# Kernel tuning notes

Hardware: AMD Instinct MI355X
Metric: run time of the kernel (lower is better)

The kernel has to match this reference:

```python
import jax, jax.numpy as jnp
import numpy as np

TOP_K = 2
CAPACITY_FACTOR = 1.0


def _ffn(x, w1, w2):
    # SwiGLU FFN: x [N, D], w1 [D, 2F], w2 [F, D]
    h = x @ w1
    x1, x2 = jnp.split(h, 2, axis=-1)
    return (x1 * jax.nn.silu(x2)) @ w2


def setup_inputs() -> dict:
    key = jax.random.key(0)
    ks = jax.random.split(key, 6)
    B, S, D, F, E_r, E_s = 4, 2048, 2048, 1024, 7, 1
    sc_in = 1.0 / np.sqrt(D)
    sc_mid = 1.0 / np.sqrt(F)
    return {
        "x": jax.random.normal(ks[0], (B, S, D), dtype=jnp.float32),
        "gate_w": jax.random.normal(ks[1], (D, E_r), dtype=jnp.float32) * sc_in,
        "expert_bias": jnp.zeros((E_r,), dtype=jnp.float32),
        "shared_w1": jax.random.normal(ks[2], (E_s, D, 2 * F), dtype=jnp.float32) * sc_in,
        "shared_w2": jax.random.normal(ks[3], (E_s, F, D), dtype=jnp.float32) * sc_mid,
        "routed_w1": jax.random.normal(ks[4], (E_r, D, 2 * F), dtype=jnp.float32) * sc_in,
        "routed_w2": jax.random.normal(ks[5], (E_r, F, D), dtype=jnp.float32) * sc_mid,
    }


def reference(x, gate_w, expert_bias, shared_w1, shared_w2, routed_w1, routed_w2):
    B, S, D = x.shape
    E_r = gate_w.shape[1]
    T = B * S
    capacity = max(1, int(CAPACITY_FACTOR * T / E_r))
    flat_x = x.reshape(T, D)

    # shared experts: applied to every token, summed
    shared_sum = jax.vmap(_ffn, in_axes=(None, 0, 0))(flat_x, shared_w1, shared_w2).sum(0)

    # gating (eval mode: no noise, no dropout)
    gate_logits = flat_x @ gate_w + expert_bias  # [T, E_r]
    aff = jax.nn.sigmoid(gate_logits)
    _, topk_idx = jax.lax.top_k(aff, TOP_K)  # [T, K]
    # mask[t, e] = expert e is among token t's top-k
    mask = (topk_idx[:, :, None] == jnp.arange(E_r)[None, None, :]).any(axis=1)  # [T, E_r]

    # per-expert capacity selection: keep top-`capacity` masked tokens by affinity
    score = jnp.where(mask, aff, -1.0).T  # [E_r, T]; aff >= 0 so -1 sorts last
    _, sel_idx = jax.lax.top_k(score, capacity)  # [E_r, capacity] token ids
    kept = jnp.take_along_axis(mask.T, sel_idx, axis=1)  # [E_r, cap]
    w = jnp.where(kept, jnp.take_along_axis(aff.T, sel_idx, axis=1), 0.0)  # [E_r, cap]

    # grouped gather -> FFN -> weighted scatter-add
    inp = flat_x[sel_idx]  # [E_r, cap, D]
    out = jax.vmap(_ffn)(inp, routed_w1, routed_w2)  # [E_r, cap, D]
    routed_sum = jnp.zeros_like(flat_x).at[sel_idx].add(out * w[:, :, None])

    return (shared_sum + routed_sum).reshape(B, S, D)
```

## Files before the change

### kernel.cpp

```cpp
#include <hip/hip_runtime.h>
#include <hip/hip_bf16.h>

typedef unsigned long long u64;
typedef __bf16 bf16x8 __attribute__((ext_vector_type(8)));
typedef float f32x4 __attribute__((ext_vector_type(4)));
typedef unsigned short ushort8_t __attribute__((ext_vector_type(8)));

#define TOKS 8192
#define DMODEL 2048
#define FD 1024
#define NEXP 7
#define CAP 1170
#define CAPP 1280

#define MFMA16(a, b, c) __builtin_amdgcn_mfma_f32_16x16x32_bf16(a, b, c, 0, 0, 0)

__device__ __forceinline__ unsigned short f2bf(float f) {
  __hip_bfloat16 b = __float2bfloat16(f);
  return __builtin_bit_cast(unsigned short, b);
}
__device__ __forceinline__ float bf2f(unsigned short u) {
  __hip_bfloat16 b = __builtin_bit_cast(__hip_bfloat16, u);
  return __bfloat162float(b);
}
__device__ __forceinline__ void gload_lds16(const void* g, void* l) {
  __builtin_amdgcn_global_load_lds(
      (const __attribute__((address_space(1))) void*)g,
      (__attribute__((address_space(3))) void*)l, 16, 0, 0);
}

__global__ void k_convert_x(const float* __restrict__ x,
                            unsigned short* __restrict__ xb, long n4) {
  long i = (long)blockIdx.x * blockDim.x + threadIdx.x;
  long stride = (long)gridDim.x * blockDim.x;
  for (; i < n4; i += stride) {
    float4 v = ((const float4*)x)[i];
    ushort4 o;
    o.x = f2bf(v.x); o.y = f2bf(v.y); o.z = f2bf(v.z); o.w = f2bf(v.w);
    ((ushort4*)xb)[i] = o;
  }
}

template <bool PERM>
__global__ void k_transpose_bf16(const float* __restrict__ in0,
                                 const float* __restrict__ inr,
                                 unsigned short* __restrict__ out,
                                 int R, int C) {
  __shared__ float tile[32][33];
  int z = blockIdx.z;
  const float* in = (z == 0) ? in0 : (inr + (long)(z - 1) * R * C);
  unsigned short* o = out + (long)z * R * C;
  int c0 = blockIdx.x * 32;
  int r0 = blockIdx.y * 32;
  int tx = threadIdx.x, ty = threadIdx.y;
#pragma unroll
  for (int k = 0; k < 4; ++k)
    tile[ty + 8 * k][tx] = in[(long)(r0 + ty + 8 * k) * C + c0 + tx];
  __syncthreads();
#pragma unroll
  for (int k = 0; k < 4; ++k) {
    int c = c0 + ty + 8 * k;
    long orow = PERM ? (long)(((c & 1023) >> 4) * 32 + ((c >> 10) << 4) + (c & 15))
                     : (long)c;
    o[orow * R + r0 + tx] = f2bf(tile[tx][ty + 8 * k]);
  }
}

__global__ void k_gating(const float* __restrict__ x,
                         const float* __restrict__ gw,
                         const float* __restrict__ bias,
                         u64* __restrict__ keys) {
  int wave = threadIdx.x >> 6;
  int lane = threadIdx.x & 63;
  int t = blockIdx.x * 4 + wave;
  const float* xr = x + (long)t * DMODEL;
  double acc[NEXP];
#pragma unroll
  for (int e = 0; e < NEXP; ++e) acc[e] = 0.0;
  for (int i = lane; i < DMODEL; i += 64) {
    double xv = (double)xr[i];
    const float* g = gw + (long)i * NEXP;
#pragma unroll
    for (int e = 0; e < NEXP; ++e) acc[e] += xv * (double)g[e];
  }
#pragma unroll
  for (int e = 0; e < NEXP; ++e) {
    for (int off = 32; off > 0; off >>= 1)
      acc[e] += __shfl_down(acc[e], off, 64);
  }
  if (lane == 0) {
    float aff[NEXP];
#pragma unroll
    for (int e = 0; e < NEXP; ++e) {
      double lg = acc[e] + (double)bias[e];
      aff[e] = (float)(1.0 / (1.0 + exp(-lg)));
    }
    int i1 = 0;
    for (int e = 1; e < NEXP; ++e) if (aff[e] > aff[i1]) i1 = e;
    int i2 = -1;
    for (int e = 0; e < NEXP; ++e) {
      if (e == i1) continue;
      if (i2 < 0 || aff[e] > aff[i2]) i2 = e;
    }
#pragma unroll
    for (int e = 0; e < NEXP; ++e) {
      u64 key = (u64)(0xFFFFFFFFu - (unsigned)t);
      if (e == i1 || e == i2) key |= ((u64)__float_as_uint(aff[e])) << 32;
      keys[(long)e * TOKS + t] = key;
    }
  }
}

__global__ __launch_bounds__(1024) void k_select(
    const u64* __restrict__ keys, int* __restrict__ sel,
    float* __restrict__ selw, unsigned* __restrict__ cnt,
    int* __restrict__ inv) {
  __shared__ unsigned hist[256];
  __shared__ u64 s_prefix;
  __shared__ unsigned s_k;
  __shared__ unsigned s_cnt;
  const int e = blockIdx.x;
  const u64* kk = keys + (long)e * TOKS;
  const int tid = threadIdx.x;
  if (tid == 0) { s_prefix = 0; s_k = CAP; s_cnt = 0; }
  __syncthreads();
  for (int shift = 56; shift >= 0; shift -= 8) {
    if (tid < 256) hist[tid] = 0;
    __syncthreads();
    u64 pref = s_prefix;
    for (int i = tid; i < TOKS; i += 1024) {
      u64 key = kk[i];
      bool match = (shift == 56) || ((key >> (shift + 8)) == pref);
      if (match) atomicAdd(&hist[(unsigned)(key >> shift) & 255u], 1u);
    }
    __syncthreads();
    if (tid == 0) {
      unsigned k = s_k, cum = 0;
      for (int b = 255; b >= 0; --b) {
        unsigned c = hist[b];
        if (cum + c >= k) {
          s_prefix = (s_prefix << 8) | (unsigned)b;
          s_k = k - cum;
          break;
        }
        cum += c;
      }
    }
    __syncthreads();
  }
  const u64 T = s_prefix;
  for (int i = tid; i < TOKS; i += 1024) {
    u64 key = kk[i];
    if (key >= T) {
      unsigned p = atomicAdd(&s_cnt, 1u);
      int tok = (int)(0xFFFFFFFFu - (unsigned)(key & 0xFFFFFFFFull));
      unsigned vb = (unsigned)(key >> 32);
      sel[e * CAPP + p] = tok;
      selw[e * CAPP + p] = vb ? __uint_as_float(vb) : 0.0f;
      if (vb) {
        unsigned pos = atomicAdd(&cnt[tok], 1u);
        inv[tok * 2 + pos] = e * CAPP + (int)p;
      }
    }
  }
  for (int i = CAP + tid; i < CAPP; i += 1024) {
    sel[e * CAPP + i] = 0;
    selw[e * CAPP + i] = 0.0f;
  }
}

__global__ __launch_bounds__(256) void k_combine(
    float* __restrict__ out, const unsigned short* __restrict__ rout,
    const int* __restrict__ inv, const unsigned* __restrict__ cnt) {
  const int tok = blockIdx.x;
  const unsigned c = cnt[tok];
  if (c == 0) return;
  int i0 = inv[tok * 2];
  int i1 = (c > 1) ? inv[tok * 2 + 1] : -1;
  if (c > 1 && i1 < i0) { int t = i0; i0 = i1; i1 = t; }
  const int col = threadIdx.x * 8;
  float* o = out + (long)tok * DMODEL + col;
  float4 v0 = *(float4*)o;
  float4 v1 = *(float4*)(o + 4);
  ushort8_t r0 = *(const ushort8_t*)&rout[(long)i0 * DMODEL + col];
#pragma unroll
  for (int j = 0; j < 4; ++j) { v0.x; }
  v0.x += bf2f(r0[0]); v0.y += bf2f(r0[1]); v0.z += bf2f(r0[2]); v0.w += bf2f(r0[3]);
  v1.x += bf2f(r0[4]); v1.y += bf2f(r0[5]); v1.z += bf2f(r0[6]); v1.w += bf2f(r0[7]);
  if (c > 1) {
    ushort8_t r1 = *(const ushort8_t*)&rout[(long)i1 * DMODEL + col];
    v0.x += bf2f(r1[0]); v0.y += bf2f(r1[1]); v0.z += bf2f(r1[2]); v0.w += bf2f(r1[3]);
    v1.x += bf2f(r1[4]); v1.y += bf2f(r1[5]); v1.z += bf2f(r1[6]); v1.w += bf2f(r1[7]);
  }
  *(float4*)o = v0;
  *(float4*)(o + 4) = v1;
}

template <int EPI, bool GATHER>
__global__ __launch_bounds__(256, 4) void k_gemm128(
    const unsigned short* __restrict__ Abase,
    const unsigned short* __restrict__ Bbase,
    unsigned short* __restrict__ Cbf, float* __restrict__ Cf32,
    const int* __restrict__ sel, const float* __restrict__ selw,
    int N, int K, long strideA, long strideB, long strideC) {
  __shared__ unsigned short lds[2][8192];
  const int tid = threadIdx.x;
  const int w = tid >> 6;
  const int lane = tid & 63;

  long lin = blockIdx.x + (long)gridDim.x * (blockIdx.y + (long)gridDim.y * blockIdx.z);
  long nwg = (long)gridDim.x * gridDim.y * gridDim.z;
  long swz = (lin & 7) * (nwg >> 3) + (lin >> 3);
  int bx = (int)(swz % gridDim.x);
  long rem = swz / gridDim.x;
  int by = (int)(rem % gridDim.y);
  int z = (int)(rem / gridDim.y);

  const long m0 = (long)by * 128;
  const long n0 = (long)bx * 128;
  const unsigned short* A = Abase + (GATHER ? 0L : (long)z * strideA);
  const unsigned short* Bm = Bbase + (long)z * strideB;

  const int wr = w >> 1;
  const int wc = w & 1;
  const int lr = lane & 15;
  const int kq = lane >> 4;

  const int r_ = (w << 4) + (lane >> 2);
  const int p_ = lane & 3;
  const unsigned short* aSrc[2];
  const unsigned short* bSrc[2];
#pragma unroll
  for (int c = 0; c < 2; ++c) {
    int r = c * 64 + r_;
    int q = p_ ^ ((r & 3) ^ ((r >> 2) & 3));
    long ar = GATHER ? (long)sel[z * CAPP + (int)m0 + r] : (m0 + r);
    aSrc[c] = A + ar * (long)K + q * 8;
    bSrc[c] = Bm + (n0 + r) * (long)K + q * 8;
  }
  const int dst0 = tid * 8;

  auto STAGE = [&](int buf, int t) {
    const long ko = (long)t * 32;
#pragma unroll
    for (int c = 0; c < 2; ++c) {
      gload_lds16(aSrc[c] + ko, &lds[buf][c * 2048 + dst0]);
      gload_lds16(bSrc[c] + ko, &lds[buf][4096 + c * 2048 + dst0]);
    }
  };

  const int gl = (lr & 3) ^ ((lr >> 2) & 3);
  const int slot = (kq ^ gl) * 8;
  const int aRow = wr * 64 + lr;
  const int bRow = wc * 64 + lr;

  const int nk = K >> 5;

  STAGE(0, 0);
  asm volatile("s_waitcnt vmcnt(0)" ::: "memory");
  __builtin_amdgcn_sched_barrier(0);
  __builtin_amdgcn_s_barrier();
  __builtin_amdgcn_sched_barrier(0);

  f32x4 acc[4][4] = {};
  int cur = 0;

#pragma unroll 1
  for (int t = 0; t < nk; ++t) {
    if (t + 1 < nk) STAGE(cur ^ 1, t + 1);
    const unsigned short* aSeg = &lds[cur][0];
    const unsigned short* bSeg = &lds[cur][4096];
    bf16x8 af[4], bf[4];
#pragma unroll
    for (int m = 0; m < 4; ++m)
      af[m] = *(const bf16x8*)&aSeg[(aRow + m * 16) * 32 + slot];
#pragma unroll
    for (int n = 0; n < 4; ++n)
      bf[n] = *(const bf16x8*)&bSeg[(bRow + n * 16) * 32 + slot];
    asm volatile("s_waitcnt lgkmcnt(0)" ::: "memory");
    __builtin_amdgcn_sched_barrier(0);
    __builtin_amdgcn_s_setprio(1);
#pragma unroll
    for (int m = 0; m < 4; ++m)
#pragma unroll
      for (int n = 0; n < 4; ++n)
        acc[m][n] = MFMA16(af[m], bf[n], acc[m][n]);
    __builtin_amdgcn_s_setprio(0);
    asm volatile("s_waitcnt vmcnt(0)" ::: "memory");
    __builtin_amdgcn_sched_barrier(0);
    __builtin_amdgcn_s_barrier();
    __builtin_amdgcn_sched_barrier(0);
    cur ^= 1;
  }

  const int r0q = (lane >> 4) * 4;
  const int cc = lane & 15;
  const long crow0 = m0 + wr * 64;
  const long ccol0 = n0 + wc * 64;

  if (EPI == 1) {
#pragma unroll
    for (int m = 0; m < 4; ++m)
#pragma unroll
      for (int r = 0; r < 4; ++r) {
        long row = crow0 + m * 16 + r0q + r;
#pragma unroll
        for (int n = 0; n < 4; ++n)
          Cf32[row * N + ccol0 + n * 16 + cc] = acc[m][n][r];
      }
  } else if (EPI == 3) {
    unsigned short* C = Cbf + (long)z * strideC;
    const int halfN = N >> 1;
    const long gcol0 = (ccol0 >> 1);
#pragma unroll
    for (int m = 0; m < 4; ++m)
#pragma unroll
      for (int r = 0; r < 4; ++r) {
        long row = crow0 + m * 16 + r0q + r;
#pragma unroll
        for (int q = 0; q < 2; ++q) {
          float x1v = acc[m][2 * q][r];
          float x2v = acc[m][2 * q + 1][r];
          float s = x2v / (1.0f + __expf(-x2v));
          C[row * halfN + gcol0 + q * 16 + cc] = f2bf(x1v * s);
        }
      }
  } else {
#pragma unroll
    for (int m = 0; m < 4; ++m)
#pragma unroll
      for (int r = 0; r < 4; ++r) {
        int rloc = (int)crow0 + m * 16 + r0q + r;
        float wgt = selw[z * CAPP + rloc];
        unsigned short* C = Cbf + ((long)z * CAPP + rloc) * N;
#pragma unroll
        for (int n = 0; n < 4; ++n)
          C[ccol0 + n * 16 + cc] = f2bf(acc[m][n][r] * wgt);
      }
  }
}

extern "C" void kernel_launch(void* const* d_in, const int* in_sizes, int n_in,
                              void* d_out, int out_size, void* d_ws,
                              size_t ws_size, hipStream_t stream) {
  (void)in_sizes; (void)n_in; (void)out_size; (void)ws_size;
  const float* x = (const float*)d_in[0];
  const float* gw = (const float*)d_in[1];
  const float* eb = (const float*)d_in[2];
  const float* sw1 = (const float*)d_in[3];
  const float* sw2 = (const float*)d_in[4];
  const float* rw1 = (const float*)d_in[5];
  const float* rw2 = (const float*)d_in[6];
  float* out = (float*)d_out;

  char* ws = (char*)d_ws;
  size_t off = 0;
  auto alloc = [&](size_t bytes) {
    size_t o = off;
    off += (bytes + 255) & ~(size_t)255;
    return o;
  };
  unsigned short* xb  = (unsigned short*)(ws + alloc((size_t)TOKS * DMODEL * 2));
  unsigned short* w1t = (unsigned short*)(ws + alloc((size_t)8 * DMODEL * (2 * FD) * 2));
  unsigned short* w2t = (unsigned short*)(ws + alloc((size_t)8 * DMODEL * FD * 2));
  unsigned short* a_sh = (unsigned short*)(ws + alloc((size_t)TOKS * FD * 2));
  unsigned short* a_r  = (unsigned short*)(ws + alloc((size_t)NEXP * CAPP * FD * 2));
  unsigned short* r_out = (unsigned short*)(ws + alloc((size_t)NEXP * CAPP * DMODEL * 2));
  u64* keys = (u64*)(ws + alloc((size_t)NEXP * TOKS * 8));
  int* sel  = (int*)(ws + alloc((size_t)NEXP * CAPP * 4));
  float* selw = (float*)(ws + alloc((size_t)NEXP * CAPP * 4));
  unsigned* cnt = (unsigned*)(ws + alloc((size_t)TOKS * 4));
  int* inv = (int*)(ws + alloc((size_t)TOKS * 2 * 4));

  k_convert_x<<<8192, 256, 0, stream>>>(x, xb, (long)TOKS * DMODEL / 4);
  dim3 tb(32, 8);
  k_transpose_bf16<true><<<dim3(64, 64, 8), tb, 0, stream>>>(sw1, rw1, w1t, DMODEL, 2 * FD);
  k_transpose_bf16<false><<<dim3(64, 32, 8), tb, 0, stream>>>(sw2, rw2, w2t, FD, DMODEL);
  k_gating<<<TOKS / 4, 256, 0, stream>>>(x, gw, eb, keys);
  hipMemsetAsync(cnt, 0, (size_t)TOKS * 4, stream);
  k_select<<<NEXP, 1024, 0, stream>>>(keys, sel, selw, cnt, inv);
  k_gemm128<3, false><<<dim3(16, 64, 1), 256, 0, stream>>>(
      xb, w1t, a_sh, nullptr, nullptr, nullptr, 2 * FD, DMODEL, 0, 0, 0);
  k_gemm128<1, false><<<dim3(16, 64, 1), 256, 0, stream>>>(
      a_sh, w2t, nullptr, out, nullptr, nullptr, DMODEL, FD, 0, 0, 0);
  k_gemm128<3, true><<<dim3(16, CAPP / 128, NEXP), 256, 0, stream>>>(
      xb, w1t + (size_t)DMODEL * (2 * FD), a_r, nullptr, sel, nullptr, 2 * FD,
      DMODEL, 0, (long)DMODEL * (2 * FD), (long)CAPP * FD);
  k_gemm128<4, false><<<dim3(16, CAPP / 128, NEXP), 256, 0, stream>>>(
      a_r, w2t + (size_t)DMODEL * FD, r_out, nullptr, sel, selw, DMODEL, FD,
      (long)CAPP * FD, (long)DMODEL * FD, 0);
  k_combine<<<TOKS, 256, 0, stream>>>(out, r_out, inv, cnt);
}
```

Measured before the change: 518.3 us.

## Merge shared and routed FFN GEMMs into unified launches; fuse convert with gating

```diff
diff --git a/kernel.cpp b/kernel.cpp
--- a/kernel.cpp
+++ b/kernel.cpp
@@ -12,6 +12,7 @@
 #define NEXP 7
 #define CAP 1170
 #define CAPP 1280
+#define URT 134
 
 #define MFMA16(a, b, c) __builtin_amdgcn_mfma_f32_16x16x32_bf16(a, b, c, 0, 0, 0)
 
@@ -29,15 +30,61 @@
       (__attribute__((address_space(3))) void*)l, 16, 0, 0);
 }
 
-__global__ void k_convert_x(const float* __restrict__ x,
-                            unsigned short* __restrict__ xb, long n4) {
-  long i = (long)blockIdx.x * blockDim.x + threadIdx.x;
-  long stride = (long)gridDim.x * blockDim.x;
-  for (; i < n4; i += stride) {
-    float4 v = ((const float4*)x)[i];
-    ushort4 o;
-    o.x = f2bf(v.x); o.y = f2bf(v.y); o.z = f2bf(v.z); o.w = f2bf(v.w);
-    ((ushort4*)xb)[i] = o;
+__global__ __launch_bounds__(256) void k_conv_gate(
+    const float* __restrict__ x, const float* __restrict__ gw,
+    const float* __restrict__ bias, unsigned short* __restrict__ xb,
+    u64* __restrict__ keys) {
+  const int t = blockIdx.x;
+  const int tid = threadIdx.x;
+  const int lane = tid & 63, wv = tid >> 6;
+  const float* xr = x + (long)t * DMODEL;
+  const int i0 = tid * 8;
+  float4 v0 = *(const float4*)&xr[i0];
+  float4 v1 = *(const float4*)&xr[i0 + 4];
+  float xv[8] = {v0.x, v0.y, v0.z, v0.w, v1.x, v1.y, v1.z, v1.w};
+  ushort8_t o;
+#pragma unroll
+  for (int j = 0; j < 8; ++j) o[j] = f2bf(xv[j]);
+  *(ushort8_t*)&xb[(long)t * DMODEL + i0] = o;
+  double acc[NEXP];
+#pragma unroll
+  for (int e = 0; e < NEXP; ++e) acc[e] = 0.0;
+#pragma unroll
+  for (int j = 0; j < 8; ++j) {
+    const float* g = gw + (long)(i0 + j) * NEXP;
+    double xd = (double)xv[j];
+#pragma unroll
+    for (int e = 0; e < NEXP; ++e) acc[e] += xd * (double)g[e];
+  }
+#pragma unroll
+  for (int e = 0; e < NEXP; ++e)
+    for (int off = 32; off > 0; off >>= 1)
+      acc[e] += __shfl_down(acc[e], off, 64);
+  __shared__ double red[4][NEXP];
+  if (lane == 0)
+#pragma unroll
+    for (int e = 0; e < NEXP; ++e) red[wv][e] = acc[e];
+  __syncthreads();
+  if (tid == 0) {
+    float aff[NEXP];
+#pragma unroll
+    for (int e = 0; e < NEXP; ++e) {
+      double lg = red[0][e] + red[1][e] + red[2][e] + red[3][e] + (double)bias[e];
+      aff[e] = (float)(1.0 / (1.0 + exp(-lg)));
+    }
+    int i1 = 0;
+    for (int e = 1; e < NEXP; ++e) if (aff[e] > aff[i1]) i1 = e;
+    int i2 = -1;
+    for (int e = 0; e < NEXP; ++e) {
+      if (e == i1) continue;
+      if (i2 < 0 || aff[e] > aff[i2]) i2 = e;
+    }
+#pragma unroll
+    for (int e = 0; e < NEXP; ++e) {
+      u64 key = (u64)(0xFFFFFFFFu - (unsigned)t);
+      if (e == i1 || e == i2) key |= ((u64)__float_as_uint(aff[e])) << 32;
+      keys[(long)e * TOKS + t] = key;
+    }
   }
 }
 
@@ -63,51 +110,6 @@
     long orow = PERM ? (long)(((c & 1023) >> 4) * 32 + ((c >> 10) << 4) + (c & 15))
                      : (long)c;
     o[orow * R + r0 + tx] = f2bf(tile[tx][ty + 8 * k]);
-  }
-}
-
-__global__ void k_gating(const float* __restrict__ x,
-                         const float* __restrict__ gw,
-                         const float* __restrict__ bias,
-                         u64* __restrict__ keys) {
-  int wave = threadIdx.x >> 6;
-  int lane = threadIdx.x & 63;
-  int t = blockIdx.x * 4 + wave;
-  const float* xr = x + (long)t * DMODEL;
-  double acc[NEXP];
-#pragma unroll
-  for (int e = 0; e < NEXP; ++e) acc[e] = 0.0;
-  for (int i = lane; i < DMODEL; i += 64) {
-    double xv = (double)xr[i];
-    const float* g = gw + (long)i * NEXP;
-#pragma unroll
-    for (int e = 0; e < NEXP; ++e) acc[e] += xv * (double)g[e];
-  }
-#pragma unroll
-  for (int e = 0; e < NEXP; ++e) {
-    for (int off = 32; off > 0; off >>= 1)
-      acc[e] += __shfl_down(acc[e], off, 64);
-  }
-  if (lane == 0) {
-    float aff[NEXP];
-#pragma unroll
-    for (int e = 0; e < NEXP; ++e) {
-      double lg = acc[e] + (double)bias[e];
-      aff[e] = (float)(1.0 / (1.0 + exp(-lg)));
-    }
-    int i1 = 0;
-    for (int e = 1; e < NEXP; ++e) if (aff[e] > aff[i1]) i1 = e;
-    int i2 = -1;
-    for (int e = 0; e < NEXP; ++e) {
-      if (e == i1) continue;
-      if (i2 < 0 || aff[e] > aff[i2]) i2 = e;
-    }
-#pragma unroll
-    for (int e = 0; e < NEXP; ++e) {
-      u64 key = (u64)(0xFFFFFFFFu - (unsigned)t);
-      if (e == i1 || e == i2) key |= ((u64)__float_as_uint(aff[e])) << 32;
-      keys[(long)e * TOKS + t] = key;
-    }
   }
 }
 
@@ -183,8 +185,6 @@
   float4 v0 = *(float4*)o;
   float4 v1 = *(float4*)(o + 4);
   ushort8_t r0 = *(const ushort8_t*)&rout[(long)i0 * DMODEL + col];
-#pragma unroll
-  for (int j = 0; j < 4; ++j) { v0.x; }
   v0.x += bf2f(r0[0]); v0.y += bf2f(r0[1]); v0.z += bf2f(r0[2]); v0.w += bf2f(r0[3]);
   v1.x += bf2f(r0[4]); v1.y += bf2f(r0[5]); v1.z += bf2f(r0[6]); v1.w += bf2f(r0[7]);
   if (c > 1) {
@@ -196,35 +196,36 @@
   *(float4*)(o + 4) = v1;
 }
 
-template <int EPI, bool GATHER>
-__global__ __launch_bounds__(256, 4) void k_gemm128(
+template <int WHICH>
+__global__ __launch_bounds__(256, 4) void k_ffn(
     const unsigned short* __restrict__ Abase,
-    const unsigned short* __restrict__ Bbase,
-    unsigned short* __restrict__ Cbf, float* __restrict__ Cf32,
-    const int* __restrict__ sel, const float* __restrict__ selw,
-    int N, int K, long strideA, long strideB, long strideC) {
+    const unsigned short* __restrict__ Wbase,
+    unsigned short* __restrict__ a_all, float* __restrict__ out,
+    unsigned short* __restrict__ r_out,
+    const int* __restrict__ sel, const float* __restrict__ selw) {
+  constexpr int K = (WHICH == 1) ? DMODEL : FD;
+  constexpr int N = (WHICH == 1) ? 2 * FD : DMODEL;
+  constexpr int nk = K >> 5;
   __shared__ unsigned short lds[2][8192];
   const int tid = threadIdx.x;
   const int w = tid >> 6;
   const int lane = tid & 63;
 
-  long lin = blockIdx.x + (long)gridDim.x * (blockIdx.y + (long)gridDim.y * blockIdx.z);
-  long nwg = (long)gridDim.x * gridDim.y * gridDim.z;
-  long swz = (lin & 7) * (nwg >> 3) + (lin >> 3);
-  int bx = (int)(swz % gridDim.x);
-  long rem = swz / gridDim.x;
-  int by = (int)(rem % gridDim.y);
-  int z = (int)(rem / gridDim.y);
-
-  const long m0 = (long)by * 128;
+  int lin = blockIdx.x + ((int)blockIdx.y << 4);
+  int gt = (lin & 7) * 268 + (lin >> 3);
+  int ct, rt;
+  int su;
+  if (gt < 2048) { su = gt >> 7; int rr = gt & 127; ct = rr >> 3; rt = rr & 7; }
+  else           { su = 16;      int rr = gt - 2048; ct = rr / 6; rt = rr % 6; }
+  const int by_u = su * 8 + rt;
+  const int bx = ct;
+
+  int e, zw, m0l;
+  if (by_u < 64) { e = -1; zw = 0; m0l = by_u << 7; }
+  else { int q = by_u - 64; e = q / 10; zw = e + 1; m0l = (q % 10) << 7; }
+  const long crow0_u = (e < 0) ? (long)m0l : (8192 + (long)e * CAPP + m0l);
   const long n0 = (long)bx * 128;
-  const unsigned short* A = Abase + (GATHER ? 0L : (long)z * strideA);
-  const unsigned short* Bm = Bbase + (long)z * strideB;
-
-  const int wr = w >> 1;
-  const int wc = w & 1;
-  const int lr = lane & 15;
-  const int kq = lane >> 4;
+  const unsigned short* Bm = Wbase + (long)zw * N * K;
 
   const int r_ = (w << 4) + (lane >> 2);
   const int p_ = lane & 3;
@@ -232,16 +233,20 @@
   const unsigned short* bSrc[2];
 #pragma unroll
   for (int c = 0; c < 2; ++c) {
-    int r = c * 64 + r_;
-    int q = p_ ^ ((r & 3) ^ ((r >> 2) & 3));
-    long ar = GATHER ? (long)sel[z * CAPP + (int)m0 + r] : (m0 + r);
-    aSrc[c] = A + ar * (long)K + q * 8;
-    bSrc[c] = Bm + (n0 + r) * (long)K + q * 8;
+    int rsg = c * 64 + r_;
+    int q = p_ ^ ((rsg >> 1) & 3);
+    long arow;
+    if (WHICH == 1)
+      arow = (e < 0) ? (long)(m0l + rsg) : (long)sel[e * CAPP + m0l + rsg];
+    else
+      arow = crow0_u + rsg;
+    aSrc[c] = Abase + arow * (long)K + q * 8;
+    bSrc[c] = Bm + (n0 + rsg) * (long)K + q * 8;
   }
   const int dst0 = tid * 8;
 
-  auto STAGE = [&](int buf, int t) {
-    const long ko = (long)t * 32;
+  auto STAGE = [&](int buf, int kt) {
+    const long ko = (long)kt * 32;
 #pragma unroll
     for (int c = 0; c < 2; ++c) {
       gload_lds16(aSrc[c] + ko, &lds[buf][c * 2048 + dst0]);
@@ -249,12 +254,11 @@
     }
   };
 
-  const int gl = (lr & 3) ^ ((lr >> 2) & 3);
-  const int slot = (kq ^ gl) * 8;
+  const int wr = w >> 1, wc = w & 1;
+  const int lr = lane & 15, kq = lane >> 4;
+  const int slot = (kq ^ ((lr >> 1) & 3)) * 8;
   const int aRow = wr * 64 + lr;
   const int bRow = wc * 64 + lr;
-
-  const int nk = K >> 5;
 
   STAGE(0, 0);
   asm volatile("s_waitcnt vmcnt(0)" ::: "memory");
@@ -266,8 +270,8 @@
   int cur = 0;
 
 #pragma unroll 1
-  for (int t = 0; t < nk; ++t) {
-    if (t + 1 < nk) STAGE(cur ^ 1, t + 1);
+  for (int kt = 0; kt < nk; ++kt) {
+    if (kt + 1 < nk) STAGE(cur ^ 1, kt + 1);
     const unsigned short* aSeg = &lds[cur][0];
     const unsigned short* bSeg = &lds[cur][4096];
     bf16x8 af[4], bf[4];
@@ -295,48 +299,47 @@
 
   const int r0q = (lane >> 4) * 4;
   const int cc = lane & 15;
-  const long crow0 = m0 + wr * 64;
-  const long ccol0 = n0 + wc * 64;
-
-  if (EPI == 1) {
+
+  if (WHICH == 1) {
+    const long gcol0 = (n0 >> 1) + wc * 32;
 #pragma unroll
     for (int m = 0; m < 4; ++m)
 #pragma unroll
-      for (int r = 0; r < 4; ++r) {
-        long row = crow0 + m * 16 + r0q + r;
-#pragma unroll
-        for (int n = 0; n < 4; ++n)
-          Cf32[row * N + ccol0 + n * 16 + cc] = acc[m][n][r];
-      }
-  } else if (EPI == 3) {
-    unsigned short* C = Cbf + (long)z * strideC;
-    const int halfN = N >> 1;
-    const long gcol0 = (ccol0 >> 1);
-#pragma unroll
-    for (int m = 0; m < 4; ++m)
-#pragma unroll
-      for (int r = 0; r < 4; ++r) {
-        long row = crow0 + m * 16 + r0q + r;
-#pragma unroll
-        for (int q = 0; q < 2; ++q) {
-          float x1v = acc[m][2 * q][r];
-          float x2v = acc[m][2 * q + 1][r];
+      for (int rj = 0; rj < 4; ++rj) {
+        long row = crow0_u + wr * 64 + m * 16 + r0q + rj;
+#pragma unroll
+        for (int q2 = 0; q2 < 2; ++q2) {
+          float x1v = acc[m][2 * q2][rj];
+          float x2v = acc[m][2 * q2 + 1][rj];
           float s = x2v / (1.0f + __expf(-x2v));
-          C[row * halfN + gcol0 + q * 16 + cc] = f2bf(x1v * s);
+          a_all[row * FD + gcol0 + q2 * 16 + cc] = f2bf(x1v * s);
         }
       }
   } else {
-#pragma unroll
-    for (int m = 0; m < 4; ++m)
-#pragma unroll
-      for (int r = 0; r < 4; ++r) {
-        int rloc = (int)crow0 + m * 16 + r0q + r;
-        float wgt = selw[z * CAPP + rloc];
-        unsigned short* C = Cbf + ((long)z * CAPP + rloc) * N;
-#pragma unroll
-        for (int n = 0; n < 4; ++n)
-          C[ccol0 + n * 16 + cc] = f2bf(acc[m][n][r] * wgt);
-      }
+    const long ccol0 = n0 + wc * 64;
+    if (e < 0) {
+#pragma unroll
+      for (int m = 0; m < 4; ++m)
+#pragma unroll
+        for (int rj = 0; rj < 4; ++rj) {
+          long row = m0l + wr * 64 + m * 16 + r0q + rj;
+#pragma unroll
+          for (int n = 0; n < 4; ++n)
+            out[row * DMODEL + ccol0 + n * 16 + cc] = acc[m][n][rj];
+        }
+    } else {
+#pragma unroll
+      for (int m = 0; m < 4; ++m)
+#pragma unroll
+        for (int rj = 0; rj < 4; ++rj) {
+          int lrow = m0l + wr * 64 + m * 16 + r0q + rj;
+          float wgt = selw[e * CAPP + lrow];
+          unsigned short* C = r_out + ((long)e * CAPP + lrow) * DMODEL;
+#pragma unroll
+          for (int n = 0; n < 4; ++n)
+            C[ccol0 + n * 16 + cc] = f2bf(acc[m][n][rj] * wgt);
+        }
+    }
   }
 }
 
@@ -360,11 +363,10 @@
     off += (bytes + 255) & ~(size_t)255;
     return o;
   };
-  unsigned short* xb  = (unsigned short*)(ws + alloc((size_t)TOKS * DMODEL * 2));
-  unsigned short* w1t = (unsigned short*)(ws + alloc((size_t)8 * DMODEL * (2 * FD) * 2));
-  unsigned short* w2t = (unsigned short*)(ws + alloc((size_t)8 * DMODEL * FD * 2));
-  unsigned short* a_sh = (unsigned short*)(ws + alloc((size_t)TOKS * FD * 2));
-  unsigned short* a_r  = (unsigned short*)(ws + alloc((size_t)NEXP * CAPP * FD * 2));
+  unsigned short* xb    = (unsigned short*)(ws + alloc((size_t)TOKS * DMODEL * 2));
+  unsigned short* w1t   = (unsigned short*)(ws + alloc((size_t)8 * DMODEL * (2 * FD) * 2));
+  unsigned short* w2t   = (unsigned short*)(ws + alloc((size_t)8 * DMODEL * FD * 2));
+  unsigned short* a_all = (unsigned short*)(ws + alloc((size_t)(TOKS + NEXP * CAPP) * FD * 2));
   unsigned short* r_out = (unsigned short*)(ws + alloc((size_t)NEXP * CAPP * DMODEL * 2));
   u64* keys = (u64*)(ws + alloc((size_t)NEXP * TOKS * 8));
   int* sel  = (int*)(ws + alloc((size_t)NEXP * CAPP * 4));
@@ -372,22 +374,15 @@
   unsigned* cnt = (unsigned*)(ws + alloc((size_t)TOKS * 4));
   int* inv = (int*)(ws + alloc((size_t)TOKS * 2 * 4));
 
-  k_convert_x<<<8192, 256, 0, stream>>>(x, xb, (long)TOKS * DMODEL / 4);
+  k_conv_gate<<<TOKS, 256, 0, stream>>>(x, gw, eb, xb, keys);
   dim3 tb(32, 8);
   k_transpose_bf16<true><<<dim3(64, 64, 8), tb, 0, stream>>>(sw1, rw1, w1t, DMODEL, 2 * FD);
   k_transpose_bf16<false><<<dim3(64, 32, 8), tb, 0, stream>>>(sw2, rw2, w2t, FD, DMODEL);
-  k_gating<<<TOKS / 4, 256, 0, stream>>>(x, gw, eb, keys);
   hipMemsetAsync(cnt, 0, (size_t)TOKS * 4, stream);
   k_select<<<NEXP, 1024, 0, stream>>>(keys, sel, selw, cnt, inv);
-  k_gemm128<3, false><<<dim3(16, 64, 1), 256, 0, stream>>>(
-      xb, w1t, a_sh, nullptr, nullptr, nullptr, 2 * FD, DMODEL, 0, 0, 0);
-  k_gemm128<1, false><<<dim3(16, 64, 1), 256, 0, stream>>>(
-      a_sh, w2t, nullptr, out, nullptr, nullptr, DMODEL, FD, 0, 0, 0);
-  k_gemm128<3, true><<<dim3(16, CAPP / 128, NEXP), 256, 0, stream>>>(
-      xb, w1t + (size_t)DMODEL * (2 * FD), a_r, nullptr, sel, nullptr, 2 * FD,
-      DMODEL, 0, (long)DMODEL * (2 * FD), (long)CAPP * FD);
-  k_gemm128<4, false><<<dim3(16, CAPP / 128, NEXP), 256, 0, stream>>>(
-      a_r, w2t + (size_t)DMODEL * FD, r_out, nullptr, sel, selw, DMODEL, FD,
-      (long)CAPP * FD, (long)DMODEL * FD, 0);
+  k_ffn<1><<<dim3(16, URT), 256, 0, stream>>>(xb, w1t, a_all, nullptr, nullptr,
+                                              sel, nullptr);
+  k_ffn<2><<<dim3(16, URT), 256, 0, stream>>>(a_all, w2t, nullptr, out, r_out,
+                                              nullptr, selw);
   k_combine<<<TOKS, 256, 0, stream>>>(out, r_out, inv, cnt);
 }
```

Result: faster. 495.8 us (-4.3%).
